# Kernel tuning notes

Hardware: AMD Instinct MI355X
Metric: run time of the kernel (lower is better)

The kernel has to match this reference:

```python
import jax, jax.numpy as jnp
import numpy as np

B, H, I, T = 256, 1024, 1, 128  # batch, hidden, input_size, decode steps


def setup_inputs() -> dict:
    key = jax.random.key(0)
    ks = jax.random.split(key, 8)
    s_ih = 1.0 / np.sqrt(H)
    return {
        "vectors": jax.random.normal(ks[0], (B, H), dtype=jnp.float32),
        "w_ih": jax.random.normal(ks[1], (3 * H, I), dtype=jnp.float32) * s_ih,
        "w_hh": jax.random.normal(ks[2], (3 * H, H), dtype=jnp.float32) * s_ih,
        "b_ih": jax.random.normal(ks[3], (3 * H,), dtype=jnp.float32) * s_ih,
        "b_hh": jax.random.normal(ks[4], (3 * H,), dtype=jnp.float32) * s_ih,
        "w_ffn": jax.random.normal(ks[5], (I, H), dtype=jnp.float32) * s_ih,
        "b_ffn": jax.random.normal(ks[6], (I,), dtype=jnp.float32) * s_ih,
        "first_input": jnp.zeros((I,), dtype=jnp.float32),
        "seq_len": T,
    }


def _free_running(vectors, w_ih, w_hh, b_ih, b_hh, w_ffn, b_ffn, first_input, seq_len):
    batch = vectors.shape[0]
    h0 = vectors  # num_layers == 1: initial hidden = encoder vector
    x0 = jnp.broadcast_to(first_input, (batch, first_input.shape[0]))

    def step(carry, _):
        h, x = carry  # h: [B,H], x: [B,I]
        gi = x @ w_ih.T + b_ih       # [B,3H]
        gh = h @ w_hh.T + b_hh       # [B,3H]
        r = jax.nn.sigmoid(gi[:, :H] + gh[:, :H])
        z = jax.nn.sigmoid(gi[:, H:2 * H] + gh[:, H:2 * H])
        n = jnp.tanh(gi[:, 2 * H:] + r * gh[:, 2 * H:])
        h_new = (1.0 - z) * n + z * h
        y = h_new @ w_ffn.T + b_ffn  # 1x1 Conv1d == per-step linear, [B,I]
        return (h_new, y), y

    _, ys = jax.lax.scan(step, (h0, x0), None, length=seq_len)
    return jnp.transpose(ys, (1, 0, 2))  # [B, seq_len, I]


def reference(vectors, w_ih, w_hh, b_ih, b_hh, w_ffn, b_ffn, first_input, seq_len):
    return _free_running(vectors, w_ih, w_hh, b_ih, b_hh, w_ffn, b_ffn,
                         first_input, seq_len)
```

## Files before the change

### kernel.cpp

```cpp
#include <hip/hip_runtime.h>
#include <hip/hip_bf16.h>
#include <cstdint>
#include <cstddef>

#define BATCH  256
#define HID    1024
#define TSTEPS 128
#define NBLK   256
#define NTHR   512

typedef __attribute__((ext_vector_type(8))) short bf16x8;
typedef __attribute__((ext_vector_type(4))) float f32x4;

__device__ inline float bf2f(__hip_bfloat16 h) { return __bfloat162float(h); }

#define MFMA(a, b, c) __builtin_amdgcn_mfma_f32_16x16x32_bf16((a), (b), (c), 0, 0, 0)

__global__ void prep_kernel(const float* __restrict__ vectors,
                            const float* __restrict__ w_hh,
                            __hip_bfloat16* __restrict__ h0,
                            __hip_bfloat16* __restrict__ w2,
                            unsigned* __restrict__ bar)
{
    const long long stride = (long long)gridDim.x * blockDim.x;
    const long long idx = (long long)blockIdx.x * blockDim.x + threadIdx.x;

    const long long NG = 32LL * 6 * 32 * 64;
    for (long long g = idx; g < NG; g += stride) {
        const int l  = (int)(g & 63);
        const int c  = (int)((g >> 6) & 31);
        const int nj = (int)(g >> 11);
        const int n  = nj % 6;
        const int jb = nj / 6;
        const int gate = n >> 1, ch = n & 1;
        const int wrow = gate * HID + jb * 32 + ch * 16 + (l & 15);
        const int k    = c * 32 + (l >> 4) * 8;
        const float* src = w_hh + (size_t)wrow * HID + k;
        alignas(16) __hip_bfloat16 v[8];
        #pragma unroll
        for (int e = 0; e < 8; ++e) v[e] = __float2bfloat16(src[e]);
        *(bf16x8*)(w2 + g * 8) = *(const bf16x8*)v;
    }

    const long long NH = (long long)BATCH * HID;
    for (long long i = idx; i < NH; i += stride)
        h0[i] = __float2bfloat16(vectors[i]);

    for (long long i = idx; i < 1024; i += stride) bar[i] = 0u;
}

__global__ __launch_bounds__(NTHR, 2)
void gru_persistent(const float* __restrict__ vectors,
                    const float* __restrict__ w_ih,
                    const float* __restrict__ b_ih,
                    const float* __restrict__ b_hh,
                    const float* __restrict__ w_ffn,
                    const float* __restrict__ b_ffn,
                    const float* __restrict__ first_input,
                    __hip_bfloat16* __restrict__ h_a,
                    __hip_bfloat16* __restrict__ h_b,
                    const __hip_bfloat16* __restrict__ w2,
                    unsigned* __restrict__ bar,
                    float* __restrict__ out)
{
    __shared__ alignas(16) unsigned char ldsA[65536];
    __shared__ float ghp[4][3][32][36];
    __shared__ float ghy[4][32];
    __shared__ alignas(16) __hip_bfloat16 hstage[1024];
    __shared__ __hip_bfloat16 wffn_lds[1024];

    const int blk  = blockIdx.x;
    const int xcd  = blk & 7, q = blk >> 3;
    const int jblk = xcd * 4 + (q & 3);
    const int mgrp = q >> 2;
    const int m_base = mgrp * 32, j_base = jblk * 32;
    const int tid  = threadIdx.x;
    const int lane = tid & 63, wv = tid >> 6;
    const int ngrp = wv & 1, kh = wv >> 1;
    const int l15  = lane & 15, kg = lane >> 4;

    float wih_[2][3], bih_[2][3], bhh_[2][3], hreg[2];
    #pragma unroll
    for (int kk = 0; kk < 2; ++kk) {
        int i = tid + kk * NTHR;
        int b = i >> 5, jc = i & 31;
        int j = j_base + jc, brow = m_base + b;
        #pragma unroll
        for (int g = 0; g < 3; ++g) {
            wih_[kk][g] = w_ih[g * HID + j];
            bih_[kk][g] = b_ih[g * HID + j];
            bhh_[kk][g] = b_hh[g * HID + j];
        }
        hreg[kk] = vectors[(size_t)brow * HID + j];
    }
    const float x0  = first_input[0];
    const float bff = b_ffn[0];

    for (int i = tid; i < 1024; i += NTHR)
        wffn_lds[i] = __float2bfloat16(w_ffn[i]);

    bf16x8 Breg[3][8];
    {
        const bf16x8* w2f = (const bf16x8*)w2;
        #pragma unroll
        for (int nn = 0; nn < 3; ++nn)
            #pragma unroll
            for (int cc = 0; cc < 8; ++cc)
                Breg[nn][cc] =
                    w2f[((size_t)(jblk * 6 + ngrp * 3 + nn) * 32 + kh * 8 + cc) * 64 + lane];
    }

    const int swz = (l15 & 7) << 4;
    const int rb0 = l15 * 2048, rb1 = (16 + l15) * 2048;
    const bf16x8 zb = {0, 0, 0, 0, 0, 0, 0, 0};

    for (int t = 0; t <= TSTEPS; ++t) {
        if (t > 0 && wv == 0) {
            const unsigned fidx = (unsigned)(mgrp * 32 + (lane & 31));
            while (__hip_atomic_load(&bar[fidx], __ATOMIC_RELAXED,
                                     __HIP_MEMORY_SCOPE_SYSTEM) < (unsigned)t)
                __builtin_amdgcn_s_sleep(1);
        }
        __syncthreads();

        const __hip_bfloat16* hcur = (t & 1) ? h_b : h_a;
        __hip_bfloat16* hnxt = (t & 1) ? h_a : h_b;
        {
            const uint4* srcA = (const uint4*)(hcur + (size_t)m_base * HID);
            uint4 tmp[8];
            #pragma unroll
            for (int it = 0; it < 8; ++it) {
                int g = tid + it * NTHR;
                asm volatile("global_load_dwordx4 %0, %1, off sc0 sc1"
                             : "=v"(tmp[it]) : "v"(srcA + g) : "memory");
            }
            asm volatile("s_waitcnt vmcnt(0)" ::: "memory");
            #pragma unroll
            for (int it = 0; it < 8; ++it) {
                int g = tid + it * NTHR;
                int row = g >> 7, k16 = g & 127;
                int bo = row * 2048 + ((k16 << 4) ^ ((row & 7) << 4));
                *(uint4*)(ldsA + bo) = tmp[it];
            }
        }
        __syncthreads();

        if (t < TSTEPS) {
            f32x4 acc00 = {0.f,0.f,0.f,0.f}, acc01 = acc00, acc10 = acc00,
                  acc11 = acc00, acc20 = acc00, acc21 = acc00;
            f32x4 accy0 = acc00, accy1 = acc00;
            #pragma unroll
            for (int cc = 0; cc < 8; ++cc) {
                const int c = (kh << 3) + cc;
                const int colb = ((c << 6) | (kg << 4)) ^ swz;
                bf16x8 a0 = *(const bf16x8*)(ldsA + rb0 + colb);
                bf16x8 a1 = *(const bf16x8*)(ldsA + rb1 + colb);
                acc00 = MFMA(a0, Breg[0][cc], acc00);
                acc01 = MFMA(a1, Breg[0][cc], acc01);
                acc10 = MFMA(a0, Breg[1][cc], acc10);
                acc11 = MFMA(a1, Breg[1][cc], acc11);
                acc20 = MFMA(a0, Breg[2][cc], acc20);
                acc21 = MFMA(a1, Breg[2][cc], acc21);
                if (ngrp == 0 && t > 0) {
                    bf16x8 wfv = *(const bf16x8*)(wffn_lds + c * 32 + kg * 8);
                    bf16x8 wb = (l15 == 0) ? wfv : zb;
                    accy0 = MFMA(a0, wb, accy0);
                    accy1 = MFMA(a1, wb, accy1);
                }
            }
            {
                const int n0 = ngrp * 3;
                #pragma unroll
                for (int r = 0; r < 4; ++r) {
                    const int rw0 = kg * 4 + r, rw1 = 16 + kg * 4 + r;
                    ghp[kh][(n0    ) >> 1][rw0][(((n0    ) & 1) << 4) + l15] = acc00[r];
                    ghp[kh][(n0    ) >> 1][rw1][(((n0    ) & 1) << 4) + l15] = acc01[r];
                    ghp[kh][(n0 + 1) >> 1][rw0][(((n0 + 1) & 1) << 4) + l15] = acc10[r];
                    ghp[kh][(n0 + 1) >> 1][rw1][(((n0 + 1) & 1) << 4) + l15] = acc11[r];
                    ghp[kh][(n0 + 2) >> 1][rw0][(((n0 + 2) & 1) << 4) + l15] = acc20[r];
                    ghp[kh][(n0 + 2) >> 1][rw1][(((n0 + 2) & 1) << 4) + l15] = acc21[r];
                }
                if (ngrp == 0 && t > 0 && l15 == 0) {
                    #pragma unroll
                    for (int r = 0; r < 4; ++r) {
                        ghy[kh][kg * 4 + r]      = accy0[r];
                        ghy[kh][16 + kg * 4 + r] = accy1[r];
                    }
                }
            }
            __syncthreads();

            #pragma unroll
            for (int kk = 0; kk < 2; ++kk) {
                const int i = tid + kk * NTHR;
                const int b = i >> 5, jc = i & 31;
                const int brow = m_base + b;
                const float x = (t == 0) ? x0
                    : (ghy[0][b] + ghy[1][b] + ghy[2][b] + ghy[3][b] + bff);
                float ghr = bhh_[kk][0], ghz = bhh_[kk][1], ghn = bhh_[kk][2];
                #pragma unroll
                for (int p = 0; p < 4; ++p) {
                    ghr += ghp[p][0][b][jc];
                    ghz += ghp[p][1][b][jc];
                    ghn += ghp[p][2][b][jc];
                }
                const float gir = fmaf(x, wih_[kk][0], bih_[kk][0]);
                const float giz = fmaf(x, wih_[kk][1], bih_[kk][1]);
                const float gin = fmaf(x, wih_[kk][2], bih_[kk][2]);
                const float rg = 1.f / (1.f + expf(-(gir + ghr)));
                const float zg = 1.f / (1.f + expf(-(giz + ghz)));
                const float ng = tanhf(fmaf(rg, ghn, gin));
                const float hnew = (1.f - zg) * ng + zg * hreg[kk];
                hreg[kk] = hnew;
                hstage[b * 32 + jc] = __float2bfloat16(hnew);
                if (t > 0 && jblk == 0 && jc == 0)
                    out[(size_t)brow * TSTEPS + (t - 1)] = x;
            }
            __syncthreads();

            if (tid < 256) {
                const int b = tid >> 3, off = tid & 7;
                unsigned long long v =
                    *(const unsigned long long*)((const char*)hstage + b * 64 + off * 8);
                __hip_atomic_store(
                    (unsigned long long*)(hnxt + (size_t)(m_base + b) * HID + j_base + off * 4),
                    v, __ATOMIC_RELAXED, __HIP_MEMORY_SCOPE_SYSTEM);
            }
            __syncthreads();
            if (tid == 0)
                __hip_atomic_store(&bar[mgrp * 32 + jblk], (unsigned)(t + 1),
                                   __ATOMIC_RELAXED, __HIP_MEMORY_SCOPE_SYSTEM);
        } else {
            if (ngrp == 0) {
                f32x4 accy0 = {0.f,0.f,0.f,0.f}, accy1 = accy0;
                #pragma unroll
                for (int cc = 0; cc < 8; ++cc) {
                    const int c = (kh << 3) + cc;
                    const int colb = ((c << 6) | (kg << 4)) ^ swz;
                    bf16x8 a0 = *(const bf16x8*)(ldsA + rb0 + colb);
                    bf16x8 a1 = *(const bf16x8*)(ldsA + rb1 + colb);
                    bf16x8 wfv = *(const bf16x8*)(wffn_lds + c * 32 + kg * 8);
                    bf16x8 wb = (l15 == 0) ? wfv : zb;
                    accy0 = MFMA(a0, wb, accy0);
                    accy1 = MFMA(a1, wb, accy1);
                }
                if (l15 == 0) {
                    #pragma unroll
                    for (int r = 0; r < 4; ++r) {
                        ghy[kh][kg * 4 + r]      = accy0[r];
                        ghy[kh][16 + kg * 4 + r] = accy1[r];
                    }
                }
            }
            __syncthreads();
            if (jblk == 0 && tid < 32) {
                const float x = ghy[0][tid] + ghy[1][tid] + ghy[2][tid]
                              + ghy[3][tid] + bff;
                out[(size_t)(m_base + tid) * TSTEPS + (TSTEPS - 1)] = x;
            }
        }
    }
}

extern "C" void kernel_launch(void* const* d_in, const int* in_sizes, int n_in,
                              void* d_out, int out_size, void* d_ws, size_t ws_size,
                              hipStream_t stream)
{
    const float* vectors     = (const float*)d_in[0];
    const float* w_ih        = (const float*)d_in[1];
    const float* w_hh        = (const float*)d_in[2];
    const float* b_ih        = (const float*)d_in[3];
    const float* b_hh        = (const float*)d_in[4];
    const float* w_ffn       = (const float*)d_in[5];
    const float* b_ffn       = (const float*)d_in[6];
    const float* first_input = (const float*)d_in[7];
    float* out = (float*)d_out;

    char* p = (char*)d_ws;
    __hip_bfloat16* h_a = (__hip_bfloat16*)p;  p += (size_t)BATCH * HID * 2;
    __hip_bfloat16* h_b = (__hip_bfloat16*)p;  p += (size_t)BATCH * HID * 2;
    __hip_bfloat16* w2  = (__hip_bfloat16*)p;  p += 32LL * 6 * 32 * 64 * 8 * 2;
    unsigned* bar = (unsigned*)p;              p += 1024 * 4;

    prep_kernel<<<1024, 256, 0, stream>>>(vectors, w_hh, h_a, w2, bar);

    void* args[] = {
        (void*)&vectors, (void*)&w_ih, (void*)&b_ih, (void*)&b_hh,
        (void*)&w_ffn, (void*)&b_ffn, (void*)&first_input,
        (void*)&h_a, (void*)&h_b, (void*)&w2, (void*)&bar, (void*)&out
    };
    hipError_t err = hipLaunchCooperativeKernel((const void*)gru_persistent,
                               dim3(NBLK), dim3(NTHR), args, 0, stream);
    (void)err;
}
```

Measured before the change: 594.0 us.

## Split batch rows into two interleaved half-groups to overlap barrier wait with compute

```diff
diff --git a/kernel.cpp b/kernel.cpp
--- a/kernel.cpp
+++ b/kernel.cpp
@@ -12,9 +12,14 @@
 typedef __attribute__((ext_vector_type(8))) short bf16x8;
 typedef __attribute__((ext_vector_type(4))) float f32x4;
 
-__device__ inline float bf2f(__hip_bfloat16 h) { return __bfloat162float(h); }
-
 #define MFMA(a, b, c) __builtin_amdgcn_mfma_f32_16x16x32_bf16((a), (b), (c), 0, 0, 0)
+
+__device__ inline float fsigmoid(float x) {
+    return __builtin_amdgcn_rcpf(1.f + __builtin_amdgcn_exp2f(-1.44269504f * x));
+}
+__device__ inline float ftanh(float x) {
+    return 1.f - 2.f * __builtin_amdgcn_rcpf(1.f + __builtin_amdgcn_exp2f(2.88539008f * x));
+}
 
 __global__ void prep_kernel(const float* __restrict__ vectors,
                             const float* __restrict__ w_hh,
@@ -63,36 +68,33 @@
                     unsigned* __restrict__ bar,
                     float* __restrict__ out)
 {
-    __shared__ alignas(16) unsigned char ldsA[65536];
-    __shared__ float ghp[4][3][32][36];
-    __shared__ float ghy[4][32];
-    __shared__ alignas(16) __hip_bfloat16 hstage[1024];
+    __shared__ alignas(16) unsigned char ldsA[2][32768];
+    __shared__ float ghp[4][3][16][36];
+    __shared__ float ghy[4][16];
+    __shared__ alignas(16) __hip_bfloat16 hstage[512];
     __shared__ __hip_bfloat16 wffn_lds[1024];
 
     const int blk  = blockIdx.x;
-    const int xcd  = blk & 7, q = blk >> 3;
-    const int jblk = xcd * 4 + (q & 3);
-    const int mgrp = q >> 2;
-    const int m_base = mgrp * 32, j_base = jblk * 32;
+    const int jblk = blk & 31;
+    const int pair = blk >> 5;
+    const int j_base = jblk * 32;
     const int tid  = threadIdx.x;
     const int lane = tid & 63, wv = tid >> 6;
     const int ngrp = wv & 1, kh = wv >> 1;
     const int l15  = lane & 15, kg = lane >> 4;
 
-    float wih_[2][3], bih_[2][3], bhh_[2][3], hreg[2];
+    const int eb = tid >> 5, ejc = tid & 31;
+    const int ej = j_base + ejc;
+    float wih_[3];
     #pragma unroll
-    for (int kk = 0; kk < 2; ++kk) {
-        int i = tid + kk * NTHR;
-        int b = i >> 5, jc = i & 31;
-        int j = j_base + jc, brow = m_base + b;
-        #pragma unroll
-        for (int g = 0; g < 3; ++g) {
-            wih_[kk][g] = w_ih[g * HID + j];
-            bih_[kk][g] = b_ih[g * HID + j];
-            bhh_[kk][g] = b_hh[g * HID + j];
-        }
-        hreg[kk] = vectors[(size_t)brow * HID + j];
-    }
+    for (int g = 0; g < 3; ++g) wih_[g] = w_ih[g * HID + ej];
+    const float bsum0 = b_ih[ej] + b_hh[ej];
+    const float bsum1 = b_ih[HID + ej] + b_hh[HID + ej];
+    const float bin_  = b_ih[2 * HID + ej];
+    const float bhn_  = b_hh[2 * HID + ej];
+    float hreg[2];
+    hreg[0] = vectors[(size_t)(pair * 16 + eb) * HID + ej];
+    hreg[1] = vectors[(size_t)((pair + 8) * 16 + eb) * HID + ej];
     const float x0  = first_input[0];
     const float bff = b_ffn[0];
 
@@ -111,152 +113,164 @@
     }
 
     const int swz = (l15 & 7) << 4;
-    const int rb0 = l15 * 2048, rb1 = (16 + l15) * 2048;
+    const int rb0 = l15 * 2048;
     const bf16x8 zb = {0, 0, 0, 0, 0, 0, 0, 0};
 
+    {
+        const uint4* src = (const uint4*)(h_a + (size_t)pair * 16 * HID);
+        uint4 tp[4];
+        #pragma unroll
+        for (int it = 0; it < 4; ++it) {
+            asm volatile("global_load_dwordx4 %0, %1, off sc0 sc1"
+                         : "=v"(tp[it]) : "v"(src + tid + it * NTHR) : "memory");
+        }
+        asm volatile("s_waitcnt vmcnt(0)" ::: "memory");
+        #pragma unroll
+        for (int it = 0; it < 4; ++it) {
+            int g = tid + it * NTHR;
+            int row = g >> 7, k16 = g & 127;
+            *(uint4*)(&ldsA[0][0] + row * 2048 + ((k16 << 4) ^ ((row & 7) << 4))) = tp[it];
+        }
+    }
+    __syncthreads();
+
     for (int t = 0; t <= TSTEPS; ++t) {
-        if (t > 0 && wv == 0) {
-            const unsigned fidx = (unsigned)(mgrp * 32 + (lane & 31));
-            while (__hip_atomic_load(&bar[fidx], __ATOMIC_RELAXED,
-                                     __HIP_MEMORY_SCOPE_SYSTEM) < (unsigned)t)
-                __builtin_amdgcn_s_sleep(1);
-        }
-        __syncthreads();
-
-        const __hip_bfloat16* hcur = (t & 1) ? h_b : h_a;
-        __hip_bfloat16* hnxt = (t & 1) ? h_a : h_b;
-        {
-            const uint4* srcA = (const uint4*)(hcur + (size_t)m_base * HID);
-            uint4 tmp[8];
-            #pragma unroll
-            for (int it = 0; it < 8; ++it) {
-                int g = tid + it * NTHR;
-                asm volatile("global_load_dwordx4 %0, %1, off sc0 sc1"
-                             : "=v"(tmp[it]) : "v"(srcA + g) : "memory");
+        #pragma unroll
+        for (int ph = 0; ph < 2; ++ph) {
+            const int mg = ph ? (pair + 8) : pair;
+            const int mb = mg * 16;
+            const int nmg = ph ? pair : (pair + 8);
+            const int nt  = ph ? t + 1 : t;
+            const bool haveNext = !(ph == 1 && t == TSTEPS);
+
+            uint4 tp[4];
+            if (haveNext) {
+                if (lane < 32) {
+                    const unsigned* fp = &bar[nmg * 32 + lane];
+                    while (__hip_atomic_load(fp, __ATOMIC_RELAXED,
+                                             __HIP_MEMORY_SCOPE_SYSTEM) < (unsigned)nt)
+                        __builtin_amdgcn_s_sleep(1);
+                }
+                const __hip_bfloat16* hsrc = (nt & 1) ? h_b : h_a;
+                const uint4* src = (const uint4*)(hsrc + (size_t)nmg * 16 * HID);
+                #pragma unroll
+                for (int it = 0; it < 4; ++it) {
+                    asm volatile("global_load_dwordx4 %0, %1, off sc0 sc1"
+                                 : "=v"(tp[it]) : "v"(src + tid + it * NTHR) : "memory");
+                }
             }
-            asm volatile("s_waitcnt vmcnt(0)" ::: "memory");
-            #pragma unroll
-            for (int it = 0; it < 8; ++it) {
-                int g = tid + it * NTHR;
-                int row = g >> 7, k16 = g & 127;
-                int bo = row * 2048 + ((k16 << 4) ^ ((row & 7) << 4));
-                *(uint4*)(ldsA + bo) = tmp[it];
-            }
-        }
-        __syncthreads();
-
-        if (t < TSTEPS) {
-            f32x4 acc00 = {0.f,0.f,0.f,0.f}, acc01 = acc00, acc10 = acc00,
-                  acc11 = acc00, acc20 = acc00, acc21 = acc00;
-            f32x4 accy0 = acc00, accy1 = acc00;
-            #pragma unroll
-            for (int cc = 0; cc < 8; ++cc) {
-                const int c = (kh << 3) + cc;
-                const int colb = ((c << 6) | (kg << 4)) ^ swz;
-                bf16x8 a0 = *(const bf16x8*)(ldsA + rb0 + colb);
-                bf16x8 a1 = *(const bf16x8*)(ldsA + rb1 + colb);
-                acc00 = MFMA(a0, Breg[0][cc], acc00);
-                acc01 = MFMA(a1, Breg[0][cc], acc01);
-                acc10 = MFMA(a0, Breg[1][cc], acc10);
-                acc11 = MFMA(a1, Breg[1][cc], acc11);
-                acc20 = MFMA(a0, Breg[2][cc], acc20);
-                acc21 = MFMA(a1, Breg[2][cc], acc21);
-                if (ngrp == 0 && t > 0) {
-                    bf16x8 wfv = *(const bf16x8*)(wffn_lds + c * 32 + kg * 8);
-                    bf16x8 wb = (l15 == 0) ? wfv : zb;
-                    accy0 = MFMA(a0, wb, accy0);
-                    accy1 = MFMA(a1, wb, accy1);
-                }
-            }
-            {
-                const int n0 = ngrp * 3;
-                #pragma unroll
-                for (int r = 0; r < 4; ++r) {
-                    const int rw0 = kg * 4 + r, rw1 = 16 + kg * 4 + r;
-                    ghp[kh][(n0    ) >> 1][rw0][(((n0    ) & 1) << 4) + l15] = acc00[r];
-                    ghp[kh][(n0    ) >> 1][rw1][(((n0    ) & 1) << 4) + l15] = acc01[r];
-                    ghp[kh][(n0 + 1) >> 1][rw0][(((n0 + 1) & 1) << 4) + l15] = acc10[r];
-                    ghp[kh][(n0 + 1) >> 1][rw1][(((n0 + 1) & 1) << 4) + l15] = acc11[r];
-                    ghp[kh][(n0 + 2) >> 1][rw0][(((n0 + 2) & 1) << 4) + l15] = acc20[r];
-                    ghp[kh][(n0 + 2) >> 1][rw1][(((n0 + 2) & 1) << 4) + l15] = acc21[r];
-                }
-                if (ngrp == 0 && t > 0 && l15 == 0) {
-                    #pragma unroll
-                    for (int r = 0; r < 4; ++r) {
-                        ghy[kh][kg * 4 + r]      = accy0[r];
-                        ghy[kh][16 + kg * 4 + r] = accy1[r];
-                    }
-                }
-            }
-            __syncthreads();
-
-            #pragma unroll
-            for (int kk = 0; kk < 2; ++kk) {
-                const int i = tid + kk * NTHR;
-                const int b = i >> 5, jc = i & 31;
-                const int brow = m_base + b;
-                const float x = (t == 0) ? x0
-                    : (ghy[0][b] + ghy[1][b] + ghy[2][b] + ghy[3][b] + bff);
-                float ghr = bhh_[kk][0], ghz = bhh_[kk][1], ghn = bhh_[kk][2];
-                #pragma unroll
-                for (int p = 0; p < 4; ++p) {
-                    ghr += ghp[p][0][b][jc];
-                    ghz += ghp[p][1][b][jc];
-                    ghn += ghp[p][2][b][jc];
-                }
-                const float gir = fmaf(x, wih_[kk][0], bih_[kk][0]);
-                const float giz = fmaf(x, wih_[kk][1], bih_[kk][1]);
-                const float gin = fmaf(x, wih_[kk][2], bih_[kk][2]);
-                const float rg = 1.f / (1.f + expf(-(gir + ghr)));
-                const float zg = 1.f / (1.f + expf(-(giz + ghz)));
-                const float ng = tanhf(fmaf(rg, ghn, gin));
-                const float hnew = (1.f - zg) * ng + zg * hreg[kk];
-                hreg[kk] = hnew;
-                hstage[b * 32 + jc] = __float2bfloat16(hnew);
-                if (t > 0 && jblk == 0 && jc == 0)
-                    out[(size_t)brow * TSTEPS + (t - 1)] = x;
-            }
-            __syncthreads();
-
-            if (tid < 256) {
-                const int b = tid >> 3, off = tid & 7;
-                unsigned long long v =
-                    *(const unsigned long long*)((const char*)hstage + b * 64 + off * 8);
-                __hip_atomic_store(
-                    (unsigned long long*)(hnxt + (size_t)(m_base + b) * HID + j_base + off * 4),
-                    v, __ATOMIC_RELAXED, __HIP_MEMORY_SCOPE_SYSTEM);
-            }
-            __syncthreads();
-            if (tid == 0)
-                __hip_atomic_store(&bar[mgrp * 32 + jblk], (unsigned)(t + 1),
-                                   __ATOMIC_RELAXED, __HIP_MEMORY_SCOPE_SYSTEM);
-        } else {
-            if (ngrp == 0) {
-                f32x4 accy0 = {0.f,0.f,0.f,0.f}, accy1 = accy0;
+
+            if (t < TSTEPS) {
+                f32x4 acc0 = {0.f,0.f,0.f,0.f}, acc1 = acc0, acc2 = acc0, accy = acc0;
+                const unsigned char* base = &ldsA[ph][0];
                 #pragma unroll
                 for (int cc = 0; cc < 8; ++cc) {
                     const int c = (kh << 3) + cc;
                     const int colb = ((c << 6) | (kg << 4)) ^ swz;
-                    bf16x8 a0 = *(const bf16x8*)(ldsA + rb0 + colb);
-                    bf16x8 a1 = *(const bf16x8*)(ldsA + rb1 + colb);
-                    bf16x8 wfv = *(const bf16x8*)(wffn_lds + c * 32 + kg * 8);
-                    bf16x8 wb = (l15 == 0) ? wfv : zb;
-                    accy0 = MFMA(a0, wb, accy0);
-                    accy1 = MFMA(a1, wb, accy1);
-                }
-                if (l15 == 0) {
+                    bf16x8 a0 = *(const bf16x8*)(base + rb0 + colb);
+                    acc0 = MFMA(a0, Breg[0][cc], acc0);
+                    acc1 = MFMA(a0, Breg[1][cc], acc1);
+                    acc2 = MFMA(a0, Breg[2][cc], acc2);
+                    if (ngrp == 0 && t > 0) {
+                        bf16x8 wfv = *(const bf16x8*)(wffn_lds + c * 32 + kg * 8);
+                        bf16x8 wb = (l15 == 0) ? wfv : zb;
+                        accy = MFMA(a0, wb, accy);
+                    }
+                }
+                {
+                    const int n0 = ngrp * 3;
                     #pragma unroll
                     for (int r = 0; r < 4; ++r) {
-                        ghy[kh][kg * 4 + r]      = accy0[r];
-                        ghy[kh][16 + kg * 4 + r] = accy1[r];
-                    }
-                }
-            }
-            __syncthreads();
-            if (jblk == 0 && tid < 32) {
-                const float x = ghy[0][tid] + ghy[1][tid] + ghy[2][tid]
-                              + ghy[3][tid] + bff;
-                out[(size_t)(m_base + tid) * TSTEPS + (TSTEPS - 1)] = x;
+                        const int rw = kg * 4 + r;
+                        ghp[kh][(n0    ) >> 1][rw][(((n0    ) & 1) << 4) + l15] = acc0[r];
+                        ghp[kh][(n0 + 1) >> 1][rw][(((n0 + 1) & 1) << 4) + l15] = acc1[r];
+                        ghp[kh][(n0 + 2) >> 1][rw][(((n0 + 2) & 1) << 4) + l15] = acc2[r];
+                    }
+                    if (ngrp == 0 && t > 0 && l15 == 0) {
+                        #pragma unroll
+                        for (int r = 0; r < 4; ++r) ghy[kh][kg * 4 + r] = accy[r];
+                    }
+                }
+                __syncthreads();
+
+                {
+                    const float x = (t == 0) ? x0
+                        : (ghy[0][eb] + ghy[1][eb] + ghy[2][eb] + ghy[3][eb] + bff);
+                    float ghr = bsum0, ghz = bsum1, ghn = bhn_;
+                    #pragma unroll
+                    for (int p = 0; p < 4; ++p) {
+                        ghr += ghp[p][0][eb][ejc];
+                        ghz += ghp[p][1][eb][ejc];
+                        ghn += ghp[p][2][eb][ejc];
+                    }
+                    const float rg = fsigmoid(fmaf(x, wih_[0], ghr));
+                    const float zg = fsigmoid(fmaf(x, wih_[1], ghz));
+                    const float gin = fmaf(x, wih_[2], bin_);
+                    const float ng = ftanh(fmaf(rg, ghn, gin));
+                    const float hnew = (1.f - zg) * ng + zg * hreg[ph];
+                    hreg[ph] = hnew;
+                    hstage[eb * 32 + ejc] = __float2bfloat16(hnew);
+                    if (t > 0 && jblk == 0 && ejc == 0)
+                        out[(size_t)(mb + eb) * TSTEPS + (t - 1)] = x;
+                }
+                __syncthreads();
+
+                __hip_bfloat16* hnxt = (t & 1) ? h_a : h_b;
+                if (tid < 128) {
+                    const int b = tid >> 3, off = tid & 7;
+                    unsigned long long v =
+                        *(const unsigned long long*)((const char*)hstage + b * 64 + off * 8);
+                    __hip_atomic_store(
+                        (unsigned long long*)(hnxt + (size_t)(mb + b) * HID + j_base + off * 4),
+                        v, __ATOMIC_RELAXED, __HIP_MEMORY_SCOPE_SYSTEM);
+                }
+                __syncthreads();
+                if (tid == 0)
+                    __hip_atomic_store(&bar[mg * 32 + jblk], (unsigned)(t + 1),
+                                       __ATOMIC_RELAXED, __HIP_MEMORY_SCOPE_SYSTEM);
+                if (haveNext) {
+                    #pragma unroll
+                    for (int it = 0; it < 4; ++it) {
+                        int g = tid + it * NTHR;
+                        int row = g >> 7, k16 = g & 127;
+                        *(uint4*)(&ldsA[ph ^ 1][0] + row * 2048 +
+                                  ((k16 << 4) ^ ((row & 7) << 4))) = tp[it];
+                    }
+                }
+                __syncthreads();
+            } else {
+                if (ngrp == 0) {
+                    f32x4 accy = {0.f,0.f,0.f,0.f};
+                    const unsigned char* base = &ldsA[ph][0];
+                    #pragma unroll
+                    for (int cc = 0; cc < 8; ++cc) {
+                        const int c = (kh << 3) + cc;
+                        const int colb = ((c << 6) | (kg << 4)) ^ swz;
+                        bf16x8 a0 = *(const bf16x8*)(base + rb0 + colb);
+                        bf16x8 wfv = *(const bf16x8*)(wffn_lds + c * 32 + kg * 8);
+                        bf16x8 wb = (l15 == 0) ? wfv : zb;
+                        accy = MFMA(a0, wb, accy);
+                    }
+                    if (l15 == 0) {
+                        #pragma unroll
+                        for (int r = 0; r < 4; ++r) ghy[kh][kg * 4 + r] = accy[r];
+                    }
+                }
+                __syncthreads();
+                if (jblk == 0 && tid < 16)
+                    out[(size_t)(mb + tid) * TSTEPS + (TSTEPS - 1)] =
+                        ghy[0][tid] + ghy[1][tid] + ghy[2][tid] + ghy[3][tid] + bff;
+                __syncthreads();
+                if (haveNext) {
+                    #pragma unroll
+                    for (int it = 0; it < 4; ++it) {
+                        int g = tid + it * NTHR;
+                        int row = g >> 7, k16 = g & 127;
+                        *(uint4*)(&ldsA[ph ^ 1][0] + row * 2048 +
+                                  ((k16 << 4) ^ ((row & 7) << 4))) = tp[it];
+                    }
+                }
+                __syncthreads();
             }
         }
     }
```

Result: slower. 667.8 us (+12.4%).

## Load hidden-state fragments directly to registers, drop LDS staging and per-wave barrier waits

Applied to the files above, without the earlier changes.

```diff
diff --git a/kernel.cpp b/kernel.cpp
--- a/kernel.cpp
+++ b/kernel.cpp
@@ -12,9 +12,14 @@
 typedef __attribute__((ext_vector_type(8))) short bf16x8;
 typedef __attribute__((ext_vector_type(4))) float f32x4;
 
-__device__ inline float bf2f(__hip_bfloat16 h) { return __bfloat162float(h); }
-
 #define MFMA(a, b, c) __builtin_amdgcn_mfma_f32_16x16x32_bf16((a), (b), (c), 0, 0, 0)
+
+__device__ inline float fsigmoid(float x) {
+    return __builtin_amdgcn_rcpf(1.f + __builtin_amdgcn_exp2f(-1.44269504f * x));
+}
+__device__ inline float ftanh(float x) {
+    return 1.f - 2.f * __builtin_amdgcn_rcpf(1.f + __builtin_amdgcn_exp2f(2.88539008f * x));
+}
 
 __global__ void prep_kernel(const float* __restrict__ vectors,
                             const float* __restrict__ w_hh,
@@ -63,35 +68,30 @@
                     unsigned* __restrict__ bar,
                     float* __restrict__ out)
 {
-    __shared__ alignas(16) unsigned char ldsA[65536];
     __shared__ float ghp[4][3][32][36];
     __shared__ float ghy[4][32];
-    __shared__ alignas(16) __hip_bfloat16 hstage[1024];
     __shared__ __hip_bfloat16 wffn_lds[1024];
 
     const int blk  = blockIdx.x;
-    const int xcd  = blk & 7, q = blk >> 3;
-    const int jblk = xcd * 4 + (q & 3);
-    const int mgrp = q >> 2;
+    const int mgrp = blk >> 5, jblk = blk & 31;
     const int m_base = mgrp * 32, j_base = jblk * 32;
     const int tid  = threadIdx.x;
     const int lane = tid & 63, wv = tid >> 6;
     const int ngrp = wv & 1, kh = wv >> 1;
     const int l15  = lane & 15, kg = lane >> 4;
 
-    float wih_[2][3], bih_[2][3], bhh_[2][3], hreg[2];
+    const int eb = tid >> 4, ejc0 = (tid & 15) * 2;
+    float wih_[2][3], bsA[2], bsB[2], bin_[2], bhn_[2], hreg[2];
     #pragma unroll
-    for (int kk = 0; kk < 2; ++kk) {
-        int i = tid + kk * NTHR;
-        int b = i >> 5, jc = i & 31;
-        int j = j_base + jc, brow = m_base + b;
-        #pragma unroll
-        for (int g = 0; g < 3; ++g) {
-            wih_[kk][g] = w_ih[g * HID + j];
-            bih_[kk][g] = b_ih[g * HID + j];
-            bhh_[kk][g] = b_hh[g * HID + j];
-        }
-        hreg[kk] = vectors[(size_t)brow * HID + j];
+    for (int e = 0; e < 2; ++e) {
+        const int j = j_base + ejc0 + e;
+        #pragma unroll
+        for (int g = 0; g < 3; ++g) wih_[e][g] = w_ih[g * HID + j];
+        bsA[e] = b_ih[j] + b_hh[j];
+        bsB[e] = b_ih[HID + j] + b_hh[HID + j];
+        bin_[e] = b_ih[2 * HID + j];
+        bhn_[e] = b_hh[2 * HID + j];
+        hreg[e] = vectors[(size_t)(m_base + eb) * HID + j];
     }
     const float x0  = first_input[0];
     const float bff = b_ffn[0];
@@ -109,41 +109,31 @@
                 Breg[nn][cc] =
                     w2f[((size_t)(jblk * 6 + ngrp * 3 + nn) * 32 + kh * 8 + cc) * 64 + lane];
     }
-
-    const int swz = (l15 & 7) << 4;
-    const int rb0 = l15 * 2048, rb1 = (16 + l15) * 2048;
+    __syncthreads();
+
     const bf16x8 zb = {0, 0, 0, 0, 0, 0, 0, 0};
+    const size_t abase = (size_t)(m_base + l15) * HID + kh * 256 + kg * 8;
 
     for (int t = 0; t <= TSTEPS; ++t) {
-        if (t > 0 && wv == 0) {
-            const unsigned fidx = (unsigned)(mgrp * 32 + (lane & 31));
-            while (__hip_atomic_load(&bar[fidx], __ATOMIC_RELAXED,
+        if (t > 0 && lane < 8) {
+            const unsigned* fp = &bar[mgrp * 32 + kh * 8 + lane];
+            while (__hip_atomic_load(fp, __ATOMIC_RELAXED,
                                      __HIP_MEMORY_SCOPE_SYSTEM) < (unsigned)t)
                 __builtin_amdgcn_s_sleep(1);
         }
-        __syncthreads();
-
-        const __hip_bfloat16* hcur = (t & 1) ? h_b : h_a;
-        __hip_bfloat16* hnxt = (t & 1) ? h_a : h_b;
-        {
-            const uint4* srcA = (const uint4*)(hcur + (size_t)m_base * HID);
-            uint4 tmp[8];
+
+        const __hip_bfloat16* hsrc = (t & 1) ? h_b : h_a;
+        bf16x8 afr[2][8];
+        #pragma unroll
+        for (int mt = 0; mt < 2; ++mt)
             #pragma unroll
-            for (int it = 0; it < 8; ++it) {
-                int g = tid + it * NTHR;
+            for (int cc = 0; cc < 8; ++cc) {
+                const __hip_bfloat16* ap = hsrc + abase + mt * 16 * HID + cc * 32;
                 asm volatile("global_load_dwordx4 %0, %1, off sc0 sc1"
-                             : "=v"(tmp[it]) : "v"(srcA + g) : "memory");
-            }
-            asm volatile("s_waitcnt vmcnt(0)" ::: "memory");
-            #pragma unroll
-            for (int it = 0; it < 8; ++it) {
-                int g = tid + it * NTHR;
-                int row = g >> 7, k16 = g & 127;
-                int bo = row * 2048 + ((k16 << 4) ^ ((row & 7) << 4));
-                *(uint4*)(ldsA + bo) = tmp[it];
-            }
-        }
-        __syncthreads();
+                             : "=v"(afr[mt][cc]) : "v"(ap) : "memory");
+            }
+        asm volatile("s_waitcnt vmcnt(0)" ::: "memory");
+        __builtin_amdgcn_sched_barrier(0);
 
         if (t < TSTEPS) {
             f32x4 acc00 = {0.f,0.f,0.f,0.f}, acc01 = acc00, acc10 = acc00,
@@ -151,10 +141,8 @@
             f32x4 accy0 = acc00, accy1 = acc00;
             #pragma unroll
             for (int cc = 0; cc < 8; ++cc) {
-                const int c = (kh << 3) + cc;
-                const int colb = ((c << 6) | (kg << 4)) ^ swz;
-                bf16x8 a0 = *(const bf16x8*)(ldsA + rb0 + colb);
-                bf16x8 a1 = *(const bf16x8*)(ldsA + rb1 + colb);
+                bf16x8 a0 = afr[0][cc];
+                bf16x8 a1 = afr[1][cc];
                 acc00 = MFMA(a0, Breg[0][cc], acc00);
                 acc01 = MFMA(a1, Breg[0][cc], acc01);
                 acc10 = MFMA(a0, Breg[1][cc], acc10);
@@ -162,7 +150,7 @@
                 acc20 = MFMA(a0, Breg[2][cc], acc20);
                 acc21 = MFMA(a1, Breg[2][cc], acc21);
                 if (ngrp == 0 && t > 0) {
-                    bf16x8 wfv = *(const bf16x8*)(wffn_lds + c * 32 + kg * 8);
+                    bf16x8 wfv = *(const bf16x8*)(wffn_lds + (kh * 8 + cc) * 32 + kg * 8);
                     bf16x8 wb = (l15 == 0) ? wfv : zb;
                     accy0 = MFMA(a0, wb, accy0);
                     accy1 = MFMA(a1, wb, accy1);
@@ -190,41 +178,36 @@
             }
             __syncthreads();
 
-            #pragma unroll
-            for (int kk = 0; kk < 2; ++kk) {
-                const int i = tid + kk * NTHR;
-                const int b = i >> 5, jc = i & 31;
-                const int brow = m_base + b;
+            __hip_bfloat16* hnxt = (t & 1) ? h_a : h_b;
+            {
                 const float x = (t == 0) ? x0
-                    : (ghy[0][b] + ghy[1][b] + ghy[2][b] + ghy[3][b] + bff);
-                float ghr = bhh_[kk][0], ghz = bhh_[kk][1], ghn = bhh_[kk][2];
+                    : (ghy[0][eb] + ghy[1][eb] + ghy[2][eb] + ghy[3][eb] + bff);
+                unsigned pack = 0;
                 #pragma unroll
-                for (int p = 0; p < 4; ++p) {
-                    ghr += ghp[p][0][b][jc];
-                    ghz += ghp[p][1][b][jc];
-                    ghn += ghp[p][2][b][jc];
-                }
-                const float gir = fmaf(x, wih_[kk][0], bih_[kk][0]);
-                const float giz = fmaf(x, wih_[kk][1], bih_[kk][1]);
-                const float gin = fmaf(x, wih_[kk][2], bih_[kk][2]);
-                const float rg = 1.f / (1.f + expf(-(gir + ghr)));
-                const float zg = 1.f / (1.f + expf(-(giz + ghz)));
-                const float ng = tanhf(fmaf(rg, ghn, gin));
-                const float hnew = (1.f - zg) * ng + zg * hreg[kk];
-                hreg[kk] = hnew;
-                hstage[b * 32 + jc] = __float2bfloat16(hnew);
-                if (t > 0 && jblk == 0 && jc == 0)
-                    out[(size_t)brow * TSTEPS + (t - 1)] = x;
-            }
-            __syncthreads();
-
-            if (tid < 256) {
-                const int b = tid >> 3, off = tid & 7;
-                unsigned long long v =
-                    *(const unsigned long long*)((const char*)hstage + b * 64 + off * 8);
+                for (int e = 0; e < 2; ++e) {
+                    const int jc = ejc0 + e;
+                    float ghr = bsA[e], ghz = bsB[e], ghn = bhn_[e];
+                    #pragma unroll
+                    for (int p = 0; p < 4; ++p) {
+                        ghr += ghp[p][0][eb][jc];
+                        ghz += ghp[p][1][eb][jc];
+                        ghn += ghp[p][2][eb][jc];
+                    }
+                    const float rg = fsigmoid(fmaf(x, wih_[e][0], ghr));
+                    const float zg = fsigmoid(fmaf(x, wih_[e][1], ghz));
+                    const float gin = fmaf(x, wih_[e][2], bin_[e]);
+                    const float ng = ftanh(fmaf(rg, ghn, gin));
+                    const float hnew = (1.f - zg) * ng + zg * hreg[e];
+                    hreg[e] = hnew;
+                    const unsigned hb =
+                        (unsigned)__builtin_bit_cast(unsigned short, __float2bfloat16(hnew));
+                    pack |= hb << (16 * e);
+                }
                 __hip_atomic_store(
-                    (unsigned long long*)(hnxt + (size_t)(m_base + b) * HID + j_base + off * 4),
-                    v, __ATOMIC_RELAXED, __HIP_MEMORY_SCOPE_SYSTEM);
+                    (unsigned*)(hnxt + (size_t)(m_base + eb) * HID + j_base + ejc0),
+                    pack, __ATOMIC_RELAXED, __HIP_MEMORY_SCOPE_SYSTEM);
+                if (t > 0 && jblk == 0 && (tid & 15) == 0)
+                    out[(size_t)(m_base + eb) * TSTEPS + (t - 1)] = x;
             }
             __syncthreads();
             if (tid == 0)
@@ -235,14 +218,10 @@
                 f32x4 accy0 = {0.f,0.f,0.f,0.f}, accy1 = accy0;
                 #pragma unroll
                 for (int cc = 0; cc < 8; ++cc) {
-                    const int c = (kh << 3) + cc;
-                    const int colb = ((c << 6) | (kg << 4)) ^ swz;
-                    bf16x8 a0 = *(const bf16x8*)(ldsA + rb0 + colb);
-                    bf16x8 a1 = *(const bf16x8*)(ldsA + rb1 + colb);
-                    bf16x8 wfv = *(const bf16x8*)(wffn_lds + c * 32 + kg * 8);
+                    bf16x8 wfv = *(const bf16x8*)(wffn_lds + (kh * 8 + cc) * 32 + kg * 8);
                     bf16x8 wb = (l15 == 0) ? wfv : zb;
-                    accy0 = MFMA(a0, wb, accy0);
-                    accy1 = MFMA(a1, wb, accy1);
+                    accy0 = MFMA(afr[0][cc], wb, accy0);
+                    accy1 = MFMA(afr[1][cc], wb, accy1);
                 }
                 if (l15 == 0) {
                     #pragma unroll
@@ -253,11 +232,9 @@
                 }
             }
             __syncthreads();
-            if (jblk == 0 && tid < 32) {
-                const float x = ghy[0][tid] + ghy[1][tid] + ghy[2][tid]
-                              + ghy[3][tid] + bff;
-                out[(size_t)(m_base + tid) * TSTEPS + (TSTEPS - 1)] = x;
-            }
+            if (jblk == 0 && tid < 32)
+                out[(size_t)(m_base + tid) * TSTEPS + (TSTEPS - 1)] =
+                    ghy[0][tid] + ghy[1][tid] + ghy[2][tid] + ghy[3][tid] + bff;
         }
     }
 }
```

Result: slower. 833.6 us (+40.3%).
